# Kernel optimization log

Hardware: AMD Instinct MI355X
Metric: run time of the kernel (lower is better)

## Reference

```python
import jax, jax.numpy as jnp
import numpy as np

B, N, D, H = 8, 1024, 1024, 16
DH = D // H
EPS = 1e-5


def setup_inputs() -> dict:
    key = jax.random.key(0)
    ks = jax.random.split(key, 12)
    s = 0.02
    return {
        "k": jax.random.normal(ks[0], (B, N, D), jnp.float32),
        "q": jax.random.normal(ks[1], (B, N, D), jnp.float32),
        "r": jax.random.normal(ks[2], (B, N, D), jnp.float32),
        "Wk": jax.random.normal(ks[3], (D, D), jnp.float32) * s,
        "bk": jnp.zeros((D,), jnp.float32),
        "Wq": jax.random.normal(ks[4], (D, D), jnp.float32) * s,
        "bq": jnp.zeros((D,), jnp.float32),
        "Wv": jax.random.normal(ks[5], (D, D), jnp.float32) * s,
        "bv": jnp.zeros((D,), jnp.float32),
        "Wo": jax.random.normal(ks[6], (D, D), jnp.float32) * s,
        "bo": jnp.zeros((D,), jnp.float32),
        "g1": jnp.ones((D,), jnp.float32),
        "b1": jnp.zeros((D,), jnp.float32),
        "g2": jnp.ones((D,), jnp.float32),
        "b2": jnp.zeros((D,), jnp.float32),
    }


def _layer_norm(x, g, b):
    mu = jnp.mean(x, axis=-1, keepdims=True)
    var = jnp.mean(jnp.square(x - mu), axis=-1, keepdims=True)
    return (x - mu) * jax.lax.rsqrt(var + EPS) * g + b


def reference(k, q, r, Wk, bk, Wq, bq, Wv, bv, Wo, bo, g1, b1, g2, b2):
    # linear projections (torch Linear: x @ W.T + b)
    kh = (k @ Wk.T + bk).reshape(B, -1, H, DH).transpose(0, 2, 1, 3)  # [B,H,Nk,DH]
    qh = (q @ Wq.T + bq).reshape(B, -1, H, DH).transpose(0, 2, 1, 3)  # [B,H,Nq,DH]
    vh = (r @ Wv.T + bv).reshape(B, -1, H, DH).transpose(0, 2, 1, 3)  # [B,H,Nk,DH]
    scale = 1.0 / jnp.sqrt(jnp.float32(DH))
    scores = jnp.einsum('bhid,bhjd->bhij', qh, kh) * scale  # [B,H,Nq,Nk]
    attn = jax.nn.softmax(scores, axis=-1)
    o = jnp.einsum('bhij,bhjd->bhid', attn, vh)  # [B,H,Nq,DH]
    o = o.transpose(0, 2, 1, 3).reshape(B, -1, D)
    mha = o @ Wo.T + bo
    residual = _layer_norm(mha + q, g1, b1)
    # source bug: mlp = nn.ReLU(BatchLinear(...)) -> mlp is plain ReLU
    out = _layer_norm(jax.nn.relu(residual) + residual, g2, b2)
    return out
```

## Files before the change

kernel.cpp:

```cpp
#include <hip/hip_runtime.h>
#include <hip/hip_bf16.h>
#include <math.h>

#define BB 8
#define NN 1024
#define DD 1024
#define HH 16
#define DH 64
#define MTOK 8192

typedef __attribute__((ext_vector_type(8))) short short8;
typedef __attribute__((ext_vector_type(4))) short short4v;
typedef __attribute__((ext_vector_type(4))) float float4v;

#define SCL_Q 0.18033688011112042f

__device__ __forceinline__ ushort f2bf(float f) {
    union { float f; unsigned u; } v; v.f = f;
    unsigned r = v.u + 0x7fffu + ((v.u >> 16) & 1u);
    return (ushort)(r >> 16);
}

__device__ __forceinline__ unsigned pkbf2(float a, float b) {
    union { float f; unsigned u; } x, y; x.f = a; y.f = b;
    return __builtin_amdgcn_perm(y.u + 0x8000u, x.u + 0x8000u, 0x07060302u);
}

__device__ __forceinline__ void gl_lds16(const ushort* g, ushort* l) {
    __builtin_amdgcn_global_load_lds(
        (const __attribute__((address_space(1))) void*)g,
        (__attribute__((address_space(3))) void*)l, 16, 0, 0);
}

__device__ __forceinline__ void stage8f_sw(const float* __restrict__ p, ushort* d) {
    float4v a = *(const float4v*)p;
    float4v b = *(const float4v*)(p + 4);
    uint4 w;
    w.x = pkbf2(a[0], a[1]); w.y = pkbf2(a[2], a[3]);
    w.z = pkbf2(b[0], b[1]); w.w = pkbf2(b[2], b[3]);
    *(uint4*)d = w;
}

struct CvtArgs {
    const float* src[7];
    ushort* dst[7];
    int n[7];
};
__global__ __launch_bounds__(256) void cvt_bf16(CvtArgs a) {
    const int z = blockIdx.y;
    const int idx = (blockIdx.x * 256 + threadIdx.x) * 8;
    if (idx >= a.n[z]) return;
    const float* s = a.src[z];
    float4v x0 = *(const float4v*)(s + idx);
    float4v x1 = *(const float4v*)(s + idx + 4);
    short8 o;
    o[0]=(short)f2bf(x0[0]); o[1]=(short)f2bf(x0[1]); o[2]=(short)f2bf(x0[2]); o[3]=(short)f2bf(x0[3]);
    o[4]=(short)f2bf(x1[0]); o[5]=(short)f2bf(x1[1]); o[6]=(short)f2bf(x1[2]); o[7]=(short)f2bf(x1[3]);
    *(short8*)(a.dst[z] + idx) = o;
}

template <typename TA, typename TW, int MODE>
__device__ __forceinline__ void gemm_core(const void* Ap, const void* Wp,
                                          const float* __restrict__ bias,
                                          void* __restrict__ outp, float oscale,
                                          ushort* As, ushort* Bs) {
    constexpr bool A_BF = (sizeof(TA) == 2);
    constexpr bool W_BF = (sizeof(TW) == 2);

    const int tid  = threadIdx.x;
    const int wid  = tid >> 6;
    const int lane = tid & 63;
    const int quad = lane >> 4;
    const int l15  = lane & 15;
    const int wr   = wid >> 1;
    const int wc   = wid & 1;
    const int m0   = blockIdx.x * 128;
    const int n0   = blockIdx.y * 128;
    const int sw   = l15 & 7;

    float4v acc[4][4] = {};

    for (int kt = 0; kt < 16; ++kt) {
        const int k0 = kt * 64;
        if constexpr (A_BF) {
            const ushort* A = (const ushort*)Ap;
            #pragma unroll
            for (int t = 0; t < 4; ++t) {
                int chunk = t * 4 + wid;
                int row   = chunk * 8 + (lane >> 3);
                int kc    = ((lane & 7) ^ (lane >> 3)) * 8;
                gl_lds16(A + (size_t)(m0 + row) * 1024 + k0 + kc, As + chunk * 512);
            }
        } else {
            const float* A = (const float*)Ap;
            #pragma unroll
            for (int i = 0; i < 4; ++i) {
                int cidx = i * 256 + tid;
                int row  = cidx >> 3;
                int cc   = cidx & 7;
                int swc  = cc ^ (row & 7);
                stage8f_sw(A + (size_t)(m0 + row) * 1024 + k0 + cc * 8,
                           &As[row * 64 + swc * 8]);
            }
        }
        if constexpr (W_BF) {
            const ushort* W = (const ushort*)Wp;
            #pragma unroll
            for (int t = 0; t < 4; ++t) {
                int chunk = t * 4 + wid;
                int row   = chunk * 8 + (lane >> 3);
                int kc    = ((lane & 7) ^ (lane >> 3)) * 8;
                gl_lds16(W + (size_t)(n0 + row) * 1024 + k0 + kc, Bs + chunk * 512);
            }
        } else {
            const float* W = (const float*)Wp;
            #pragma unroll
            for (int i = 0; i < 4; ++i) {
                int cidx = i * 256 + tid;
                int row  = cidx >> 3;
                int cc   = cidx & 7;
                int swc  = cc ^ (row & 7);
                stage8f_sw(W + (size_t)(n0 + row) * 1024 + k0 + cc * 8,
                           &Bs[row * 64 + swc * 8]);
            }
        }
        __syncthreads();

        #pragma unroll
        for (int kk = 0; kk < 2; ++kk) {
            short8 af[4], bfr[4];
            #pragma unroll
            for (int i = 0; i < 4; ++i)
                af[i] = *(const short8*)&As[(wr * 64 + i * 16 + l15) * 64 +
                                            ((kk * 4 + quad) ^ sw) * 8];
            #pragma unroll
            for (int j = 0; j < 4; ++j)
                bfr[j] = *(const short8*)&Bs[(wc * 64 + j * 16 + l15) * 64 +
                                             ((kk * 4 + quad) ^ sw) * 8];
            #pragma unroll
            for (int i = 0; i < 4; ++i)
                #pragma unroll
                for (int j = 0; j < 4; ++j) {
                    if constexpr (MODE == 1)
                        acc[i][j] = __builtin_amdgcn_mfma_f32_16x16x32_bf16(af[i], bfr[j], acc[i][j], 0, 0, 0);
                    else
                        acc[j][i] = __builtin_amdgcn_mfma_f32_16x16x32_bf16(bfr[j], af[i], acc[j][i], 0, 0, 0);
                }
        }
        __syncthreads();
    }

    if constexpr (MODE == 1) {
        ushort* out = (ushort*)outp;
        #pragma unroll
        for (int j = 0; j < 4; ++j) {
            const int col = n0 + wc * 64 + j * 16 + l15;
            const float bv = bias[col];
            const int h = col >> 6;
            const int d = col & 63;
            #pragma unroll
            for (int i = 0; i < 4; ++i) {
                const int rowbase = m0 + wr * 64 + i * 16 + quad * 4;
                int bi = rowbase >> 10, n = rowbase & 1023;
                uint2 w;
                w.x = pkbf2(acc[i][j][0] + bv, acc[i][j][1] + bv);
                w.y = pkbf2(acc[i][j][2] + bv, acc[i][j][3] + bv);
                *(uint2*)&out[(((size_t)(bi * HH + h) * DH + d) * NN) + n] = w;
            }
        }
    } else {
        #pragma unroll
        for (int p = 0; p < 4; ++p) {
            const int fb = n0 + wc * 64 + p * 16 + quad * 4;
            const float4v bv4 = *(const float4v*)&bias[fb];
            const int h = fb >> 6;
            const int d = fb & 63;
            #pragma unroll
            for (int q = 0; q < 4; ++q) {
                const int tok = m0 + wr * 64 + q * 16 + l15;
                if constexpr (MODE == 0) {
                    ushort* out = (ushort*)outp;
                    int bi = tok >> 10, n = tok & 1023;
                    uint2 w;
                    w.x = pkbf2((acc[p][q][0] + bv4[0]) * oscale,
                                (acc[p][q][1] + bv4[1]) * oscale);
                    w.y = pkbf2((acc[p][q][2] + bv4[2]) * oscale,
                                (acc[p][q][3] + bv4[3]) * oscale);
                    *(uint2*)&out[(((size_t)(bi * HH + h) * NN + n) * DH) + d] = w;
                } else {
                    float* out = (float*)outp;
                    float4v ov;
                    #pragma unroll
                    for (int r = 0; r < 4; ++r) ov[r] = acc[p][q][r] + bv4[r];
                    *(float4v*)&out[(size_t)tok * 1024 + fb] = ov;
                }
            }
        }
    }
}

template <typename TA, typename TW>
__global__ __launch_bounds__(256) void proj3(const void* q, const void* k, const void* r,
                                             const void* Wq, const void* Wk, const void* Wv,
                                             const float* bq, const float* bk, const float* bv,
                                             ushort* qh, ushort* kh, ushort* vt) {
    __shared__ ushort As[128 * 64];
    __shared__ ushort Bs[128 * 64];
    if (blockIdx.z == 0)      gemm_core<TA, TW, 0>(q, Wq, bq, qh, SCL_Q, As, Bs);
    else if (blockIdx.z == 1) gemm_core<TA, TW, 0>(k, Wk, bk, kh, 1.0f, As, Bs);
    else                      gemm_core<TA, TW, 1>(r, Wv, bv, vt, 1.0f, As, Bs);
}

template <typename TA, typename TW>
__global__ __launch_bounds__(256) void gemm_out(const void* A, const void* W,
                                                const float* bias, float* out) {
    __shared__ ushort As[128 * 64];
    __shared__ ushort Bs[128 * 64];
    gemm_core<TA, TW, 2>(A, W, bias, out, 1.0f, As, Bs);
}

__global__ __launch_bounds__(256) void attn_fused(const ushort* __restrict__ qh,
                                                  const ushort* __restrict__ kh,
                                                  const ushort* __restrict__ vt,
                                                  ushort* __restrict__ o) {
    __shared__ ushort Ks[64 * 64];
    __shared__ ushort Vs[64 * 64];
    __shared__ ushort Ps[4][2][16 * 72];

    const int tid  = threadIdx.x;
    const int wid  = tid >> 6;
    const int lane = tid & 63;
    const int quad = lane >> 4;
    const int l15  = lane & 15;
    const int sw   = l15 & 7;
    const int bh   = blockIdx.x;
    const int qt   = blockIdx.y;
    const int h    = bh & 15;
    const int b    = bh >> 4;

    const ushort* qb = qh + (size_t)bh * NN * DH;
    const ushort* kb = kh + (size_t)bh * NN * DH;
    const ushort* vb = vt + (size_t)bh * DH * NN;

    short8 qf[2][2];
    #pragma unroll
    for (int u = 0; u < 2; ++u) {
        const int qrow = qt * 128 + wid * 32 + u * 16 + l15;
        qf[u][0] = *(const short8*)(qb + (size_t)qrow * DH + quad * 8);
        qf[u][1] = *(const short8*)(qb + (size_t)qrow * DH + 32 + quad * 8);
    }

    float lsum[2] = {0.f, 0.f};
    float4v oaccT[2][4] = {};

    for (int kt = 0; kt < 16; ++kt) {
        #pragma unroll
        for (int t = 0; t < 2; ++t) {
            int chunk = t * 4 + wid;
            int row   = chunk * 8 + (lane >> 3);
            int kc    = ((lane & 7) ^ (lane >> 3)) * 8;
            gl_lds16(kb + (size_t)(kt * 64 + row) * DH + kc, Ks + chunk * 512);
            gl_lds16(vb + (size_t)row * NN + kt * 64 + kc, Vs + chunk * 512);
        }
        __syncthreads();

        float4v sacc[2][4] = {};
        #pragma unroll
        for (int s = 0; s < 2; ++s)
            #pragma unroll
            for (int c = 0; c < 4; ++c) {
                short8 kf = *(const short8*)&Ks[(c * 16 + l15) * 64 + ((s * 4 + quad) ^ sw) * 8];
                #pragma unroll
                for (int u = 0; u < 2; ++u)
                    sacc[u][c] = __builtin_amdgcn_mfma_f32_16x16x32_bf16(kf, qf[u][s], sacc[u][c], 0, 0, 0);
            }

        #pragma unroll
        for (int u = 0; u < 2; ++u)
            #pragma unroll
            for (int c = 0; c < 4; ++c) {
                float p0 = exp2f(sacc[u][c][0]);
                float p1 = exp2f(sacc[u][c][1]);
                float p2 = exp2f(sacc[u][c][2]);
                float p3 = exp2f(sacc[u][c][3]);
                lsum[u] += (p0 + p1) + (p2 + p3);
                uint2 w;
                w.x = pkbf2(p0, p1);
                w.y = pkbf2(p2, p3);
                *(uint2*)&Ps[wid][u][l15 * 72 + c * 16 + quad * 4] = w;
            }

        #pragma unroll
        for (int s = 0; s < 2; ++s) {
            short8 pf[2];
            #pragma unroll
            for (int u = 0; u < 2; ++u)
                pf[u] = *(const short8*)&Ps[wid][u][l15 * 72 + s * 32 + quad * 8];
            #pragma unroll
            for (int nn = 0; nn < 4; ++nn) {
                short8 vf = *(const short8*)&Vs[(nn * 16 + l15) * 64 + ((s * 4 + quad) ^ sw) * 8];
                #pragma unroll
                for (int u = 0; u < 2; ++u)
                    oaccT[u][nn] = __builtin_amdgcn_mfma_f32_16x16x32_bf16(vf, pf[u], oaccT[u][nn], 0, 0, 0);
            }
        }
        __syncthreads();
    }

    #pragma unroll
    for (int u = 0; u < 2; ++u) {
        float t = lsum[u];
        t += __shfl_xor(t, 16);
        t += __shfl_xor(t, 32);
        float inv = 1.0f / t;
        int row = qt * 128 + wid * 32 + u * 16 + l15;
        size_t base = ((size_t)b * NN + row) * DD + h * 64 + quad * 4;
        #pragma unroll
        for (int nn = 0; nn < 4; ++nn) {
            uint2 w;
            w.x = pkbf2(oaccT[u][nn][0] * inv, oaccT[u][nn][1] * inv);
            w.y = pkbf2(oaccT[u][nn][2] * inv, oaccT[u][nn][3] * inv);
            *(uint2*)&o[base + nn * 16] = w;
        }
    }
}

__global__ __launch_bounds__(256) void ln_fuse(const float* __restrict__ mha,
                                               const float* __restrict__ q,
                                               const float* __restrict__ g1,
                                               const float* __restrict__ b1,
                                               const float* __restrict__ g2,
                                               const float* __restrict__ b2,
                                               float* __restrict__ out) {
    __shared__ float red1[8];
    __shared__ float red2[8];
    const int tid  = threadIdx.x;
    const int wid  = tid >> 6;
    const int lane = tid & 63;
    const size_t base = (size_t)blockIdx.x * 1024 + tid * 4;

    float4v xv = *(const float4v*)(mha + base);
    float4v qv = *(const float4v*)(q + base);
    float x[4];
    float s = 0.f, ss = 0.f;
    for (int i = 0; i < 4; ++i) {
        x[i] = xv[i] + qv[i];
        s += x[i]; ss += x[i] * x[i];
    }
    for (int off = 1; off < 64; off <<= 1) {
        s += __shfl_xor(s, off); ss += __shfl_xor(ss, off);
    }
    if (lane == 0) { red1[wid * 2] = s; red1[wid * 2 + 1] = ss; }
    __syncthreads();
    s  = red1[0] + red1[2] + red1[4] + red1[6];
    ss = red1[1] + red1[3] + red1[5] + red1[7];
    float mu = s * (1.0f / 1024.0f);
    float rstd = rsqrtf(ss * (1.0f / 1024.0f) - mu * mu + 1e-5f);

    float4v g1v = *(const float4v*)(g1 + tid * 4);
    float4v b1v = *(const float4v*)(b1 + tid * 4);
    float y[4];
    float s2 = 0.f, ss2 = 0.f;
    for (int i = 0; i < 4; ++i) {
        float rr = (x[i] - mu) * rstd * g1v[i] + b1v[i];
        y[i] = fmaxf(rr, 0.f) + rr;
        s2 += y[i]; ss2 += y[i] * y[i];
    }
    for (int off = 1; off < 64; off <<= 1) {
        s2 += __shfl_xor(s2, off); ss2 += __shfl_xor(ss2, off);
    }
    if (lane == 0) { red2[wid * 2] = s2; red2[wid * 2 + 1] = ss2; }
    __syncthreads();
    s2  = red2[0] + red2[2] + red2[4] + red2[6];
    ss2 = red2[1] + red2[3] + red2[5] + red2[7];
    float mu2 = s2 * (1.0f / 1024.0f);
    float rstd2 = rsqrtf(ss2 * (1.0f / 1024.0f) - mu2 * mu2 + 1e-5f);

    float4v g2v = *(const float4v*)(g2 + tid * 4);
    float4v b2v = *(const float4v*)(b2 + tid * 4);
    float4v ov;
    for (int i = 0; i < 4; ++i) ov[i] = (y[i] - mu2) * rstd2 * g2v[i] + b2v[i];
    *(float4v*)(out + base) = ov;
}

extern "C" void kernel_launch(void* const* d_in, const int* in_sizes, int n_in,
                              void* d_out, int out_size, void* d_ws, size_t ws_size,
                              hipStream_t stream) {
    const float* k  = (const float*)d_in[0];
    const float* q  = (const float*)d_in[1];
    const float* r  = (const float*)d_in[2];
    const float* Wk = (const float*)d_in[3];
    const float* bk = (const float*)d_in[4];
    const float* Wq = (const float*)d_in[5];
    const float* bq = (const float*)d_in[6];
    const float* Wv = (const float*)d_in[7];
    const float* bv = (const float*)d_in[8];
    const float* Wo = (const float*)d_in[9];
    const float* bo = (const float*)d_in[10];
    const float* g1 = (const float*)d_in[11];
    const float* b1 = (const float*)d_in[12];
    const float* g2 = (const float*)d_in[13];
    const float* b2 = (const float*)d_in[14];

    char* ws = (char*)d_ws;
    const size_t MB = 1u << 20;
    dim3 blk(256);

    if (ws_size >= 73 * MB) {
        ushort* qh  = (ushort*)(ws);
        ushort* kh  = (ushort*)(ws + 16 * MB);
        ushort* vt  = (ushort*)(ws + 32 * MB);
        ushort* ob  = (ushort*)(ws + 48 * MB);
        ushort* Wqc = (ushort*)(ws + 64 * MB);
        ushort* Wkc = (ushort*)(ws + 66 * MB);
        ushort* Wvc = (ushort*)(ws + 68 * MB);
        ushort* Woc = (ushort*)(ws + 70 * MB);
        float*  mh  = (float*)(ws);

        CvtArgs ca;
        ca.src[0] = Wq; ca.dst[0] = Wqc; ca.n[0] = DD * DD;
        ca.src[1] = Wk; ca.dst[1] = Wkc; ca.n[1] = DD * DD;
        ca.src[2] = Wv; ca.dst[2] = Wvc; ca.n[2] = DD * DD;
        ca.src[3] = Wo; ca.dst[3] = Woc; ca.n[3] = DD * DD;
        for (int i = 4; i < 7; ++i) { ca.src[i] = Wq; ca.dst[i] = Wqc; ca.n[i] = 0; }
        cvt_bf16<<<dim3(512, 4), blk, 0, stream>>>(ca);

        proj3<float, ushort><<<dim3(64, 8, 3), blk, 0, stream>>>(
            q, k, r, Wqc, Wkc, Wvc, bq, bk, bv, qh, kh, vt);
        attn_fused<<<dim3(HH * BB, 8), blk, 0, stream>>>(qh, kh, vt, ob);
        gemm_out<ushort, ushort><<<dim3(64, 8), blk, 0, stream>>>(ob, Woc, bo, mh);
        ln_fuse<<<dim3(MTOK), blk, 0, stream>>>(mh, q, g1, b1, g2, b2, (float*)d_out);
    } else {
        ushort* qh  = (ushort*)(ws);
        ushort* kh  = (ushort*)(ws + 16 * MB);
        ushort* vt  = (ushort*)(ws + 32 * MB);
        ushort* ob  = (ushort*)(ws + 48 * MB);
        ushort* Wqc = (ushort*)(ws + 48 * MB);
        ushort* Wkc = (ushort*)(ws + 50 * MB);
        ushort* Wvc = (ushort*)(ws + 52 * MB);
        float*  mh  = (float*)(ws);

        CvtArgs ca;
        ca.src[0] = Wq; ca.dst[0] = Wqc; ca.n[0] = DD * DD;
        ca.src[1] = Wk; ca.dst[1] = Wkc; ca.n[1] = DD * DD;
        ca.src[2] = Wv; ca.dst[2] = Wvc; ca.n[2] = DD * DD;
        for (int i = 3; i < 7; ++i) { ca.src[i] = Wq; ca.dst[i] = Wqc; ca.n[i] = 0; }
        cvt_bf16<<<dim3(512, 3), blk, 0, stream>>>(ca);

        proj3<float, ushort><<<dim3(64, 8, 3), blk, 0, stream>>>(
            q, k, r, Wqc, Wkc, Wvc, bq, bk, bv, qh, kh, vt);
        attn_fused<<<dim3(HH * BB, 8), blk, 0, stream>>>(qh, kh, vt, ob);
        gemm_out<ushort, float><<<dim3(64, 8), blk, 0, stream>>>(ob, Wo, bo, mh);
        ln_fuse<<<dim3(MTOK), blk, 0, stream>>>(mh, q, g1, b1, g2, b2, (float*)d_out);
    }
}
```

Baseline: 367.8 us.

## Pre-convert activations to bf16 and use one wavefront per row in layernorm

The fast path now converts q, k and r activations to bf16 in the conversion kernel, alongside the weights, so the projection GEMM reads bf16 inputs instead of fp32. The workspace layout grows accordingly and the path now requires 121 MB. The layernorm kernel now handles one row per wavefront, with reductions done by shuffles only, removing the shared memory and __syncthreads. This trades an extra full read and write of the activations for half-width GEMM input loads. The fast path no longer runs if the harness workspace is smaller than 121 MB.

```diff
diff --git a/kernel.cpp b/kernel.cpp
--- a/kernel.cpp
+++ b/kernel.cpp
@@ -53,10 +53,10 @@
     const float* s = a.src[z];
     float4v x0 = *(const float4v*)(s + idx);
     float4v x1 = *(const float4v*)(s + idx + 4);
-    short8 o;
-    o[0]=(short)f2bf(x0[0]); o[1]=(short)f2bf(x0[1]); o[2]=(short)f2bf(x0[2]); o[3]=(short)f2bf(x0[3]);
-    o[4]=(short)f2bf(x1[0]); o[5]=(short)f2bf(x1[1]); o[6]=(short)f2bf(x1[2]); o[7]=(short)f2bf(x1[3]);
-    *(short8*)(a.dst[z] + idx) = o;
+    uint4 w;
+    w.x = pkbf2(x0[0], x0[1]); w.y = pkbf2(x0[2], x0[3]);
+    w.z = pkbf2(x1[0], x1[1]); w.w = pkbf2(x1[2], x1[3]);
+    *(uint4*)(a.dst[z] + idx) = w;
 }
 
 template <typename TA, typename TW, int MODE>
@@ -332,55 +332,63 @@
                                                const float* __restrict__ g2,
                                                const float* __restrict__ b2,
                                                float* __restrict__ out) {
-    __shared__ float red1[8];
-    __shared__ float red2[8];
-    const int tid  = threadIdx.x;
-    const int wid  = tid >> 6;
-    const int lane = tid & 63;
-    const size_t base = (size_t)blockIdx.x * 1024 + tid * 4;
-
-    float4v xv = *(const float4v*)(mha + base);
-    float4v qv = *(const float4v*)(q + base);
-    float x[4];
+    const int row  = blockIdx.x * 4 + (threadIdx.x >> 6);
+    const int lane = threadIdx.x & 63;
+    const float* mrow = mha + (size_t)row * 1024;
+    const float* qrow = q + (size_t)row * 1024;
+
+    float x[16];
     float s = 0.f, ss = 0.f;
-    for (int i = 0; i < 4; ++i) {
-        x[i] = xv[i] + qv[i];
-        s += x[i]; ss += x[i] * x[i];
-    }
+    #pragma unroll
+    for (int c = 0; c < 4; ++c) {
+        float4v mv = *(const float4v*)(mrow + c * 256 + lane * 4);
+        float4v qv = *(const float4v*)(qrow + c * 256 + lane * 4);
+        #pragma unroll
+        for (int i = 0; i < 4; ++i) {
+            float v = mv[i] + qv[i];
+            x[c * 4 + i] = v;
+            s += v; ss += v * v;
+        }
+    }
+    #pragma unroll
     for (int off = 1; off < 64; off <<= 1) {
         s += __shfl_xor(s, off); ss += __shfl_xor(ss, off);
     }
-    if (lane == 0) { red1[wid * 2] = s; red1[wid * 2 + 1] = ss; }
-    __syncthreads();
-    s  = red1[0] + red1[2] + red1[4] + red1[6];
-    ss = red1[1] + red1[3] + red1[5] + red1[7];
     float mu = s * (1.0f / 1024.0f);
     float rstd = rsqrtf(ss * (1.0f / 1024.0f) - mu * mu + 1e-5f);
 
-    float4v g1v = *(const float4v*)(g1 + tid * 4);
-    float4v b1v = *(const float4v*)(b1 + tid * 4);
-    float y[4];
+    float y[16];
     float s2 = 0.f, ss2 = 0.f;
-    for (int i = 0; i < 4; ++i) {
-        float rr = (x[i] - mu) * rstd * g1v[i] + b1v[i];
-        y[i] = fmaxf(rr, 0.f) + rr;
-        s2 += y[i]; ss2 += y[i] * y[i];
-    }
+    #pragma unroll
+    for (int c = 0; c < 4; ++c) {
+        float4v g1v = *(const float4v*)(g1 + c * 256 + lane * 4);
+        float4v b1v = *(const float4v*)(b1 + c * 256 + lane * 4);
+        #pragma unroll
+        for (int i = 0; i < 4; ++i) {
+            float rr = (x[c * 4 + i] - mu) * rstd * g1v[i] + b1v[i];
+            float v = fmaxf(rr, 0.f) + rr;
+            y[c * 4 + i] = v;
+            s2 += v; ss2 += v * v;
+        }
+    }
+    #pragma unroll
     for (int off = 1; off < 64; off <<= 1) {
         s2 += __shfl_xor(s2, off); ss2 += __shfl_xor(ss2, off);
     }
-    if (lane == 0) { red2[wid * 2] = s2; red2[wid * 2 + 1] = ss2; }
-    __syncthreads();
-    s2  = red2[0] + red2[2] + red2[4] + red2[6];
-    ss2 = red2[1] + red2[3] + red2[5] + red2[7];
     float mu2 = s2 * (1.0f / 1024.0f);
     float rstd2 = rsqrtf(ss2 * (1.0f / 1024.0f) - mu2 * mu2 + 1e-5f);
 
-    float4v g2v = *(const float4v*)(g2 + tid * 4);
-    float4v b2v = *(const float4v*)(b2 + tid * 4);
-    float4v ov;
-    for (int i = 0; i < 4; ++i) ov[i] = (y[i] - mu2) * rstd2 * g2v[i] + b2v[i];
-    *(float4v*)(out + base) = ov;
+    float* orow = out + (size_t)row * 1024;
+    #pragma unroll
+    for (int c = 0; c < 4; ++c) {
+        float4v g2v = *(const float4v*)(g2 + c * 256 + lane * 4);
+        float4v b2v = *(const float4v*)(b2 + c * 256 + lane * 4);
+        float4v ov;
+        #pragma unroll
+        for (int i = 0; i < 4; ++i)
+            ov[i] = (y[c * 4 + i] - mu2) * rstd2 * g2v[i] + b2v[i];
+        *(float4v*)(orow + c * 256 + lane * 4) = ov;
+    }
 }
 
 extern "C" void kernel_launch(void* const* d_in, const int* in_sizes, int n_in,
@@ -406,30 +414,35 @@
     const size_t MB = 1u << 20;
     dim3 blk(256);
 
-    if (ws_size >= 73 * MB) {
-        ushort* qh  = (ushort*)(ws);
-        ushort* kh  = (ushort*)(ws + 16 * MB);
-        ushort* vt  = (ushort*)(ws + 32 * MB);
-        ushort* ob  = (ushort*)(ws + 48 * MB);
-        ushort* Wqc = (ushort*)(ws + 64 * MB);
-        ushort* Wkc = (ushort*)(ws + 66 * MB);
-        ushort* Wvc = (ushort*)(ws + 68 * MB);
-        ushort* Woc = (ushort*)(ws + 70 * MB);
+    if (ws_size >= 121 * MB) {
+        ushort* qc  = (ushort*)(ws);
+        ushort* kc  = (ushort*)(ws + 16 * MB);
+        ushort* rc  = (ushort*)(ws + 32 * MB);
+        ushort* Wqc = (ushort*)(ws + 48 * MB);
+        ushort* Wkc = (ushort*)(ws + 50 * MB);
+        ushort* Wvc = (ushort*)(ws + 52 * MB);
+        ushort* Woc = (ushort*)(ws + 54 * MB);
+        ushort* qh  = (ushort*)(ws + 56 * MB);
+        ushort* kh  = (ushort*)(ws + 72 * MB);
+        ushort* vt  = (ushort*)(ws + 88 * MB);
+        ushort* ob  = (ushort*)(ws + 104 * MB);
         float*  mh  = (float*)(ws);
 
         CvtArgs ca;
-        ca.src[0] = Wq; ca.dst[0] = Wqc; ca.n[0] = DD * DD;
-        ca.src[1] = Wk; ca.dst[1] = Wkc; ca.n[1] = DD * DD;
-        ca.src[2] = Wv; ca.dst[2] = Wvc; ca.n[2] = DD * DD;
-        ca.src[3] = Wo; ca.dst[3] = Woc; ca.n[3] = DD * DD;
-        for (int i = 4; i < 7; ++i) { ca.src[i] = Wq; ca.dst[i] = Wqc; ca.n[i] = 0; }
-        cvt_bf16<<<dim3(512, 4), blk, 0, stream>>>(ca);
-
-        proj3<float, ushort><<<dim3(64, 8, 3), blk, 0, stream>>>(
-            q, k, r, Wqc, Wkc, Wvc, bq, bk, bv, qh, kh, vt);
+        ca.src[0] = q;  ca.dst[0] = qc;  ca.n[0] = MTOK * DD;
+        ca.src[1] = k;  ca.dst[1] = kc;  ca.n[1] = MTOK * DD;
+        ca.src[2] = r;  ca.dst[2] = rc;  ca.n[2] = MTOK * DD;
+        ca.src[3] = Wq; ca.dst[3] = Wqc; ca.n[3] = DD * DD;
+        ca.src[4] = Wk; ca.dst[4] = Wkc; ca.n[4] = DD * DD;
+        ca.src[5] = Wv; ca.dst[5] = Wvc; ca.n[5] = DD * DD;
+        ca.src[6] = Wo; ca.dst[6] = Woc; ca.n[6] = DD * DD;
+        cvt_bf16<<<dim3(4096, 7), blk, 0, stream>>>(ca);
+
+        proj3<ushort, ushort><<<dim3(64, 8, 3), blk, 0, stream>>>(
+            qc, kc, rc, Wqc, Wkc, Wvc, bq, bk, bv, qh, kh, vt);
         attn_fused<<<dim3(HH * BB, 8), blk, 0, stream>>>(qh, kh, vt, ob);
         gemm_out<ushort, ushort><<<dim3(64, 8), blk, 0, stream>>>(ob, Woc, bo, mh);
-        ln_fuse<<<dim3(MTOK), blk, 0, stream>>>(mh, q, g1, b1, g2, b2, (float*)d_out);
+        ln_fuse<<<dim3(MTOK / 4), blk, 0, stream>>>(mh, q, g1, b1, g2, b2, (float*)d_out);
     } else {
         ushort* qh  = (ushort*)(ws);
         ushort* kh  = (ushort*)(ws + 16 * MB);
@@ -451,6 +464,6 @@
             q, k, r, Wqc, Wkc, Wvc, bq, bk, bv, qh, kh, vt);
         attn_fused<<<dim3(HH * BB, 8), blk, 0, stream>>>(qh, kh, vt, ob);
         gemm_out<ushort, float><<<dim3(64, 8), blk, 0, stream>>>(ob, Wo, bo, mh);
-        ln_fuse<<<dim3(MTOK), blk, 0, stream>>>(mh, q, g1, b1, g2, b2, (float*)d_out);
-    }
-}
+        ln_fuse<<<dim3(MTOK / 4), blk, 0, stream>>>(mh, q, g1, b1, g2, b2, (float*)d_out);
+    }
+}
```

Result: faster. 351.6 us (-4.4%).
